# Kernel optimization log

Measured on AMD Instinct MI355X. Metric: run time of the kernel, lower is better.

## Reference

```python
import jax, jax.numpy as jnp
import numpy as np

B, M, N = 8, 1024, 2048          # batch, check nodes, variable nodes
NUM_ITERS = 5
ROW_DEGREE = 8                   # ones per check row (sparse Tanner graph)
NEG_BIG = -1e30 - 1.0


def _make_H():
    rng = np.random.RandomState(0)
    H = np.zeros((M, N), dtype=np.int32)
    for i in range(M):
        cols = rng.choice(N, size=ROW_DEGREE, replace=False)
        H[i, cols] = 1
    # guarantee every variable node has at least one check
    empty = np.where(H.sum(0) == 0)[0]
    for j in empty:
        H[rng.randint(M), j] = 1
    return H


def setup_inputs() -> dict:
    key = jax.random.key(0)
    k1, _ = jax.random.split(key)
    soft_input = jax.random.normal(k1, (B, N), dtype=jnp.float32) * 2.0
    check_weight = jnp.full((1,), -1.07, dtype=jnp.float32)  # NMS normalized factor
    H = jnp.asarray(_make_H())
    return {"soft_input": soft_input, "check_weight": check_weight, "H": H}


def reference(soft_input, check_weight, H):
    Hf = H.astype(jnp.float32)                      # [M, N]
    back = jnp.where(Hf == 0, NEG_BIG, 0.0)[None]   # [1, M, N]
    supp = (1.0 - Hf)[None]                         # [1, M, N]
    alpha = jax.nn.softplus(check_weight)           # NMS scalar normalization

    def body(cv, _):
        # --- variable-to-check: vc = (sum_m cv + llr) on edges, minus own message
        col_sum = jnp.sum(cv, axis=1) + soft_input            # [B, N]
        vc = col_sum[:, None, :] * Hf - cv                    # [B, M, N]
        # --- check-to-variable: min-sum with min/submin trick
        vc_abs = jnp.clip(jnp.abs(vc), 0.0, 1e30)
        dec = -vc_abs + back                                  # mask off non-edges
        top2 = jax.lax.top_k(dec, 2)[0]                       # [B, M, 2]
        mn = (-top2[..., 0])[:, :, None] * Hf                 # row min, broadcast on edges
        sub = (-top2[..., 1])[:, :, None] * Hf                # row second min
        result = jnp.where(vc_abs > mn, mn, sub)              # exclude-self min
        sign = jnp.sign(supp + vc)                            # non-edges -> sign(+1)
        row_prod = jnp.prod(sign, axis=2)[:, :, None] * Hf
        result_sign = row_prod * sign                         # product of other signs
        cv_new = result * jax.lax.stop_gradient(result_sign) * alpha
        return cv_new, None

    cv0 = jnp.zeros((soft_input.shape[0], Hf.shape[0], Hf.shape[1]), jnp.float32)
    cv_final, _ = jax.lax.scan(body, cv0, None, length=NUM_ITERS)
    soft_output = soft_input + jnp.sum(cv_final, axis=1)      # [B, N] posterior LLRs
    return soft_output
```

## Files before the change

### kernel.cpp

```cpp
#include <hip/hip_runtime.h>
#include <hip/hip_bf16.h>


#define M_CHECK 1024
#define N_VAR   2048
#define BATCH   8
#define MAXD    12
#define NUM_ITERS 5
#define FXS 16384.0f
#define FXI (1.0f / 16384.0f)

__global__ __launch_bounds__(256) void build_rows_kernel(
    const int* __restrict__ H, int* __restrict__ deg,
    int* __restrict__ row_cols_T)
{
    const int m    = blockIdx.x * 4 + (threadIdx.x >> 6);
    const int lane = threadIdx.x & 63;
    const unsigned long long below = (1ULL << lane) - 1ULL;
    const int4* __restrict__ H4 = (const int4*)(H + m * N_VAR);

    int base = 0;
    for (int c = 0; c < N_VAR; c += 256) {
        int4 h = H4[(c >> 2) + lane];
        unsigned long long m0 = __ballot(h.x != 0);
        unsigned long long m1 = __ballot(h.y != 0);
        unsigned long long m2 = __ballot(h.z != 0);
        unsigned long long m3 = __ballot(h.w != 0);
        int pb = __popcll(m0 & below) + __popcll(m1 & below)
               + __popcll(m2 & below) + __popcll(m3 & below);
        int b0 = (int)((m0 >> lane) & 1);
        int b1 = (int)((m1 >> lane) & 1);
        int b2 = (int)((m2 >> lane) & 1);
        int col = c + 4 * lane;
        int r = base + pb;
        if (h.x) { if (r < MAXD) row_cols_T[r * M_CHECK + m] = col; }
        r += b0;
        if (h.y) { if (r < MAXD) row_cols_T[r * M_CHECK + m] = col + 1; }
        r += b1;
        if (h.z) { if (r < MAXD) row_cols_T[r * M_CHECK + m] = col + 2; }
        r += b2;
        if (h.w) { if (r < MAXD) row_cols_T[r * M_CHECK + m] = col + 3; }
        base += __popcll(m0) + __popcll(m1) + __popcll(m2) + __popcll(m3);
    }
    if (lane == 0) deg[m] = (base < MAXD) ? base : MAXD;
}

#define DECODE_ITER(ACCG, ACCS, DO_RESET, ACCR)                              \
  {                                                                          \
    float vcs[MAXD];                                                         \
    float mn1 = 1e38f, mn2 = 1e38f;                                          \
    unsigned sx = 0u; bool zr = false;                                       \
    _Pragma("unroll")                                                        \
    for (int d = 0; d < MAXD; ++d) {                                         \
      vcs[d] = 0.f;                                                          \
      if (d < 8 || __any(dm > d)) {                                          \
        if (d < dm) {                                                        \
          float vc = softc[d] + (float)ACCG[cols[d]] * FXI - cv[d];          \
          vcs[d] = vc;                                                       \
          float a = fminf(fabsf(vc), 1e30f);                                 \
          if (a < mn1) { mn2 = mn1; mn1 = a; }                               \
          else if (a < mn2) { mn2 = a; }                                     \
          sx ^= (__float_as_uint(vc) & 0x80000000u);                         \
          zr |= (vc == 0.f);                                                 \
        }                                                                    \
      }                                                                      \
    }                                                                        \
    const float zmul = zr ? 0.f : alpha;                                     \
    _Pragma("unroll")                                                        \
    for (int d = 0; d < MAXD; ++d) {                                         \
      if (d < 8 || __any(dm > d)) {                                          \
        if (d < dm) {                                                        \
          float vc  = vcs[d];                                                \
          float a   = fminf(fabsf(vc), 1e30f);                               \
          float res = (a > mn1) ? mn1 : mn2;           \
          unsigned o = sx ^ (__float_as_uint(vc) & 0x80000000u);             \
          float v   = res * zmul;                                  \
          float cvn = __uint_as_float(__float_as_uint(v) ^ o);               \
          cv[d] = cvn;                                                       \
          atomicAdd(&ACCS[cols[d]], __float2int_rn(cvn * FXS));              \
        }                                                                    \
      }                                                                      \
    }                                                                        \
    if (DO_RESET) { ACCR[n0] = 0; ACCR[n1] = 0; }                            \
    __syncthreads();                                                         \
  }

__global__ __launch_bounds__(1024) void decode_kernel(
    const float* __restrict__ soft_input, const float* __restrict__ check_weight,
    const int* __restrict__ deg, const int* __restrict__ row_cols_T,
    float* __restrict__ out)
{
    __shared__ int   acc0[N_VAR];
    __shared__ int   acc1[N_VAR];
    __shared__ int   acc2[N_VAR];
    __shared__ float soft_s[N_VAR];

    const int b = blockIdx.x;
    const int t = threadIdx.x;
    const float alpha = log1pf(expf(check_weight[0]));

    const int n0 = t, n1 = t + 1024;
    const float s0 = soft_input[b * N_VAR + n0];
    const float s1 = soft_input[b * N_VAR + n1];
    soft_s[n0] = s0;  soft_s[n1] = s1;
    acc1[n0] = 0; acc1[n1] = 0;
    acc2[n0] = 0; acc2[n1] = 0;

    const int dm = deg[t];
    int cols[MAXD];
#pragma unroll
    for (int d = 0; d < MAXD; ++d)
        cols[d] = (d < dm) ? row_cols_T[d * M_CHECK + t] : 0;
    __syncthreads();

    float softc[MAXD];
#pragma unroll
    for (int d = 0; d < MAXD; ++d)
        softc[d] = (d < dm) ? soft_s[cols[d]] : 0.f;

    float cv[MAXD];

    {
        float mn1 = 1e38f, mn2 = 1e38f;
        unsigned sx = 0u; bool zr = false;
#pragma unroll
        for (int d = 0; d < MAXD; ++d) {
            if (d < 8 || __any(dm > d)) {
                if (d < dm) {
                    float vc = softc[d];
                    float a  = fminf(fabsf(vc), 1e30f);
                    if (a < mn1) { mn2 = mn1; mn1 = a; }
                    else if (a < mn2) { mn2 = a; }
                    sx ^= (__float_as_uint(vc) & 0x80000000u);
                    zr |= (vc == 0.f);
                }
            }
        }
        const float zmul = zr ? 0.f : alpha;
#pragma unroll
        for (int d = 0; d < MAXD; ++d) {
            if (d < 8 || __any(dm > d)) {
                if (d < dm) {
                    float vc  = softc[d];
                    float a   = fminf(fabsf(vc), 1e30f);
                    float res = (a > mn1) ? mn1 : mn2;
                    unsigned o = sx ^ (__float_as_uint(vc) & 0x80000000u);
                    float v   = res * zmul;
                    float cvn = __uint_as_float(__float_as_uint(v) ^ o);
                    cv[d] = cvn;
                    atomicAdd(&acc1[cols[d]], __float2int_rn(cvn * FXS));
                }
            }
        }
    }
    __syncthreads();

    DECODE_ITER(acc1, acc2, true,  acc0)
    DECODE_ITER(acc2, acc0, true,  acc1)
    DECODE_ITER(acc0, acc1, true,  acc2)
    DECODE_ITER(acc1, acc2, false, acc0)

    out[b * N_VAR + n0] = s0 + (float)acc2[n0] * FXI;
    out[b * N_VAR + n1] = s1 + (float)acc2[n1] * FXI;
}

extern "C" void kernel_launch(void* const* d_in, const int* in_sizes, int n_in,
                              void* d_out, int out_size, void* d_ws, size_t ws_size,
                              hipStream_t stream)
{
    const float* soft_input   = (const float*)d_in[0];
    const float* check_weight = (const float*)d_in[1];
    const int*   H            = (const int*)d_in[2];
    float*       out          = (float*)d_out;

    int* deg        = (int*)d_ws;
    int* row_cols_T = deg + M_CHECK;

    build_rows_kernel<<<M_CHECK / 4, 256, 0, stream>>>(H, deg, row_cols_T);
    decode_kernel<<<BATCH, 1024, 0, stream>>>(
        soft_input, check_weight, deg, row_cols_T, out);
}
```

Baseline: 21.68 us.

## Sort check rows by degree so full warps take an unpredicated degree-8 path

The row-building kernel now stages column indices in shared memory and uses a global atomic counter to put degree-8 rows at the front and other rows at the back of the row table. The decode kernel checks whether a whole wavefront holds degree-8 rows and, if so, runs a fixed 8-edge loop with no predicates or __any votes; otherwise it runs the general predicated path. It also removes the 1e30 clamp and folds the first iteration into the shared macro. The cost is an extra memset launch and atomics in the preprocessing step, and row order now depends on atomic arrival order.

Measured after the change: 36.84 us. 70.0% more time.

```diff
diff --git a/kernel.cpp b/kernel.cpp
--- a/kernel.cpp
+++ b/kernel.cpp
@@ -11,11 +11,15 @@
 #define FXI (1.0f / 16384.0f)
 
 __global__ __launch_bounds__(256) void build_rows_kernel(
-    const int* __restrict__ H, int* __restrict__ deg,
-    int* __restrict__ row_cols_T)
+    const int* __restrict__ H, int* __restrict__ cnt,
+    int* __restrict__ deg, int* __restrict__ row_cols_T)
 {
-    const int m    = blockIdx.x * 4 + (threadIdx.x >> 6);
+    __shared__ int stage[4][MAXD];
+    __shared__ int info[4][2];
+
+    const int w    = threadIdx.x >> 6;
     const int lane = threadIdx.x & 63;
+    const int m    = blockIdx.x * 4 + w;
     const unsigned long long below = (1ULL << lane) - 1ULL;
     const int4* __restrict__ H4 = (const int4*)(H + m * N_VAR);
 
@@ -33,62 +37,77 @@
         int b2 = (int)((m2 >> lane) & 1);
         int col = c + 4 * lane;
         int r = base + pb;
-        if (h.x) { if (r < MAXD) row_cols_T[r * M_CHECK + m] = col; }
+        if (h.x) { if (r < MAXD) stage[w][r] = col; }
         r += b0;
-        if (h.y) { if (r < MAXD) row_cols_T[r * M_CHECK + m] = col + 1; }
+        if (h.y) { if (r < MAXD) stage[w][r] = col + 1; }
         r += b1;
-        if (h.z) { if (r < MAXD) row_cols_T[r * M_CHECK + m] = col + 2; }
+        if (h.z) { if (r < MAXD) stage[w][r] = col + 2; }
         r += b2;
-        if (h.w) { if (r < MAXD) row_cols_T[r * M_CHECK + m] = col + 3; }
+        if (h.w) { if (r < MAXD) stage[w][r] = col + 3; }
         base += __popcll(m0) + __popcll(m1) + __popcll(m2) + __popcll(m3);
     }
-    if (lane == 0) deg[m] = (base < MAXD) ? base : MAXD;
+
+    if (lane == 0) {
+        int degc = (base < MAXD) ? base : MAXD;
+        int is8  = (degc == 8) ? 1 : 0;
+        int pos  = atomicAdd(&cnt[is8 ? 0 : 1], 1);
+        int nid  = is8 ? pos : (M_CHECK - 1 - pos);
+        deg[nid] = degc;
+        info[w][0] = nid;
+        info[w][1] = degc;
+    }
+    __syncthreads();
+
+    const int nid  = info[w][0];
+    const int degc = info[w][1];
+    if (lane < degc)
+        row_cols_T[lane * M_CHECK + nid] = stage[w][lane];
 }
 
-#define DECODE_ITER(ACCG, ACCS, DO_RESET, ACCR)                              \
+#define ROW_BODY(DLIM, PRED, ACCG, ACCS, PEEL)                               \
   {                                                                          \
     float vcs[MAXD];                                                         \
     float mn1 = 1e38f, mn2 = 1e38f;                                          \
     unsigned sx = 0u; bool zr = false;                                       \
     _Pragma("unroll")                                                        \
-    for (int d = 0; d < MAXD; ++d) {                                         \
-      vcs[d] = 0.f;                                                          \
-      if (d < 8 || __any(dm > d)) {                                          \
-        if (d < dm) {                                                        \
-          float vc = softc[d] + (float)ACCG[cols[d]] * FXI - cv[d];          \
-          vcs[d] = vc;                                                       \
-          float a = fminf(fabsf(vc), 1e30f);                                 \
-          if (a < mn1) { mn2 = mn1; mn1 = a; }                               \
-          else if (a < mn2) { mn2 = a; }                                     \
-          sx ^= (__float_as_uint(vc) & 0x80000000u);                         \
-          zr |= (vc == 0.f);                                                 \
-        }                                                                    \
+    for (int d = 0; d < DLIM; ++d) {                                         \
+      if (!PRED || d < dm) {                                                 \
+        float vc = PEEL ? softc[d]                                           \
+                        : softc[d] + (float)ACCG[cols[d]] * FXI - cv[d];     \
+        vcs[d] = vc;                                                         \
+        float a = fabsf(vc);                                                 \
+        if (a < mn1) { mn2 = mn1; mn1 = a; }                                 \
+        else if (a < mn2) { mn2 = a; }                                       \
+        sx ^= (__float_as_uint(vc) & 0x80000000u);                           \
+        zr |= (vc == 0.f);                                                   \
       }                                                                      \
     }                                                                        \
     const float zmul = zr ? 0.f : alpha;                                     \
     _Pragma("unroll")                                                        \
-    for (int d = 0; d < MAXD; ++d) {                                         \
-      if (d < 8 || __any(dm > d)) {                                          \
-        if (d < dm) {                                                        \
-          float vc  = vcs[d];                                                \
-          float a   = fminf(fabsf(vc), 1e30f);                               \
-          float res = (a > mn1) ? mn1 : mn2;           \
-          unsigned o = sx ^ (__float_as_uint(vc) & 0x80000000u);             \
-          float v   = res * zmul;                                  \
-          float cvn = __uint_as_float(__float_as_uint(v) ^ o);               \
-          cv[d] = cvn;                                                       \
-          atomicAdd(&ACCS[cols[d]], __float2int_rn(cvn * FXS));              \
-        }                                                                    \
+    for (int d = 0; d < DLIM; ++d) {                                         \
+      if (!PRED || d < dm) {                                                 \
+        float vc  = vcs[d];                                                  \
+        float a   = fabsf(vc);                                               \
+        float res = (a > mn1) ? mn1 : mn2;             \
+        unsigned o = sx ^ (__float_as_uint(vc) & 0x80000000u);               \
+        float v   = res * zmul;                                    \
+        float cvn = __uint_as_float(__float_as_uint(v) ^ o);                 \
+        cv[d] = cvn;                                                         \
+        atomicAdd(&ACCS[cols[d]], __float2int_rn(cvn * FXS));                \
       }                                                                      \
     }                                                                        \
-    if (DO_RESET) { ACCR[n0] = 0; ACCR[n1] = 0; }                            \
-    __syncthreads();                                                         \
   }
+
+#define DECODE_ITER(ACCG, ACCS, PEEL, DO_RESET, ACCR)                        \
+  if (clean) ROW_BODY(8,    false, ACCG, ACCS, PEEL)                         \
+  else       ROW_BODY(MAXD, true,  ACCG, ACCS, PEEL)                         \
+  if (DO_RESET) { ACCR[n0] = 0; ACCR[n1] = 0; }                              \
+  __syncthreads();
 
 __global__ __launch_bounds__(1024) void decode_kernel(
     const float* __restrict__ soft_input, const float* __restrict__ check_weight,
-    const int* __restrict__ deg, const int* __restrict__ row_cols_T,
-    float* __restrict__ out)
+    const int* __restrict__ cnt, const int* __restrict__ deg,
+    const int* __restrict__ row_cols_T, float* __restrict__ out)
 {
     __shared__ int   acc0[N_VAR];
     __shared__ int   acc1[N_VAR];
@@ -106,6 +125,9 @@
     acc1[n0] = 0; acc1[n1] = 0;
     acc2[n0] = 0; acc2[n1] = 0;
 
+    const int n8 = cnt[0];
+    const bool clean = ((t | 63) < n8);
+
     const int dm = deg[t];
     int cols[MAXD];
 #pragma unroll
@@ -120,45 +142,11 @@
 
     float cv[MAXD];
 
-    {
-        float mn1 = 1e38f, mn2 = 1e38f;
-        unsigned sx = 0u; bool zr = false;
-#pragma unroll
-        for (int d = 0; d < MAXD; ++d) {
-            if (d < 8 || __any(dm > d)) {
-                if (d < dm) {
-                    float vc = softc[d];
-                    float a  = fminf(fabsf(vc), 1e30f);
-                    if (a < mn1) { mn2 = mn1; mn1 = a; }
-                    else if (a < mn2) { mn2 = a; }
-                    sx ^= (__float_as_uint(vc) & 0x80000000u);
-                    zr |= (vc == 0.f);
-                }
-            }
-        }
-        const float zmul = zr ? 0.f : alpha;
-#pragma unroll
-        for (int d = 0; d < MAXD; ++d) {
-            if (d < 8 || __any(dm > d)) {
-                if (d < dm) {
-                    float vc  = softc[d];
-                    float a   = fminf(fabsf(vc), 1e30f);
-                    float res = (a > mn1) ? mn1 : mn2;
-                    unsigned o = sx ^ (__float_as_uint(vc) & 0x80000000u);
-                    float v   = res * zmul;
-                    float cvn = __uint_as_float(__float_as_uint(v) ^ o);
-                    cv[d] = cvn;
-                    atomicAdd(&acc1[cols[d]], __float2int_rn(cvn * FXS));
-                }
-            }
-        }
-    }
-    __syncthreads();
-
-    DECODE_ITER(acc1, acc2, true,  acc0)
-    DECODE_ITER(acc2, acc0, true,  acc1)
-    DECODE_ITER(acc0, acc1, true,  acc2)
-    DECODE_ITER(acc1, acc2, false, acc0)
+    DECODE_ITER(acc0, acc1,                  true,  false, acc0)
+    DECODE_ITER(acc1, acc2,                  false, true,  acc0)
+    DECODE_ITER(acc2, acc0,                  false, true,  acc1)
+    DECODE_ITER(acc0, acc1,                  false, true,  acc2)
+    DECODE_ITER(acc1, acc2,                  false, false, acc0)
 
     out[b * N_VAR + n0] = s0 + (float)acc2[n0] * FXI;
     out[b * N_VAR + n1] = s1 + (float)acc2[n1] * FXI;
@@ -173,10 +161,12 @@
     const int*   H            = (const int*)d_in[2];
     float*       out          = (float*)d_out;
 
-    int* deg        = (int*)d_ws;
+    int* cnt        = (int*)d_ws;
+    int* deg        = cnt + 4;
     int* row_cols_T = deg + M_CHECK;
 
-    build_rows_kernel<<<M_CHECK / 4, 256, 0, stream>>>(H, deg, row_cols_T);
+    hipMemsetAsync(cnt, 0, 2 * sizeof(int), stream);
+    build_rows_kernel<<<M_CHECK / 4, 256, 0, stream>>>(H, cnt, deg, row_cols_T);
     decode_kernel<<<BATCH, 1024, 0, stream>>>(
-        soft_input, check_weight, deg, row_cols_T, out);
+        soft_input, check_weight, cnt, deg, row_cols_T, out);
 }
```
